# Optimization experiments

Measured on AMD Instinct MI355X. Metric: run time of the kernel, lower is better.

## Reference

```python
import jax, jax.numpy as jnp
import numpy as np


def setup_inputs() -> dict:
    key = jax.random.key(0)
    k1, k2 = jax.random.split(key)
    B, Q, T, D = 128, 512, 512, 256
    inputs = jax.random.normal(k1, (B, T, D), dtype=jnp.float32)
    query = jax.random.normal(k2, (B, Q, D), dtype=jnp.float32)
    return {"inputs": inputs, "query": query}


def reference(inputs, query):
    # inputs: [B, T, D] (keys == values), query: [B, Q, D]
    D = inputs.shape[2]
    scale = 1.0 / jnp.sqrt(jnp.asarray(D, dtype=inputs.dtype))
    # scores: [B, Q, T]
    scores = jnp.einsum("bqd,btd->bqt", query, inputs) * scale
    weights = jax.nn.softmax(scores, axis=2)
    # attended: [B, Q, D]
    attended = jnp.einsum("bqt,btd->bqd", weights, inputs)
    # pool over query dim -> [B, D]
    return jnp.sum(attended, axis=1)
```

## Files before the change

### kernel.cpp

```cpp
#include <hip/hip_runtime.h>
#include <hip/hip_bf16.h>


typedef __bf16 bf16x8 __attribute__((ext_vector_type(8)));
typedef float  f32x4  __attribute__((ext_vector_type(4)));

#define B_    128
#define Tn    512
#define Dn    256
#define SCALE 0.0625f

__device__ __forceinline__ int lidx(int row, int ch) {
  return row * 256 + (((ch ^ (row & 31)) & 31) << 3);
}

__device__ __forceinline__ void stage_load(const float* __restrict__ src,
                                           int tid, float4* pre) {
#pragma unroll
  for (int i = 0; i < 8; ++i) {
    int u = i * 256 + tid;
    int row = u >> 5, ch = u & 31;
    const float4* p = (const float4*)(src + row * 256 + ch * 8);
    pre[2 * i]     = p[0];
    pre[2 * i + 1] = p[1];
  }
}

__device__ __forceinline__ void stage_store(__bf16* dst, int tid,
                                            const float4* pre) {
#pragma unroll
  for (int i = 0; i < 8; ++i) {
    int u = i * 256 + tid;
    int row = u >> 5, ch = u & 31;
    float4 v0 = pre[2 * i], v1 = pre[2 * i + 1];
    bf16x8 w;
    w[0] = (__bf16)v0.x; w[1] = (__bf16)v0.y;
    w[2] = (__bf16)v0.z; w[3] = (__bf16)v0.w;
    w[4] = (__bf16)v1.x; w[5] = (__bf16)v1.y;
    w[6] = (__bf16)v1.z; w[7] = (__bf16)v1.w;
    *(bf16x8*)(dst + lidx(row, ch)) = w;
  }
}

__global__ void __launch_bounds__(256, 2) attn_qk_colsum(
    const float* __restrict__ inputs, const float* __restrict__ query,
    float* __restrict__ c_ws) {
  __shared__ __bf16 smem[2 * 64 * 256];
  __bf16* buf0 = smem;
  __bf16* buf1 = smem + 64 * 256;

  const int tid  = threadIdx.x;
  const int bidx = blockIdx.x;
  const int b  = bidx & 127;
  const int qt = bidx >> 7;

  const float* qsrc = query  + ((size_t)b * 512 + (size_t)qt * 64) * Dn;
  const float* ksrc = inputs + (size_t)b * Tn * Dn;

  const int wave = tid >> 6, lane = tid & 63;
  const int quad = lane >> 4, l15 = lane & 15;
  const int qh = wave & 1;
  const int th = wave >> 1;

  {
    float4 pre[16];
    stage_load(qsrc, tid, pre);
    stage_store(buf0, tid, pre);
  }
  __syncthreads();

  bf16x8 afrag[2][8];
#pragma unroll
  for (int m = 0; m < 2; ++m)
#pragma unroll
    for (int dc = 0; dc < 8; ++dc)
      afrag[m][dc] =
          *(const bf16x8*)(buf0 + lidx(qh * 32 + m * 16 + l15, dc * 4 + quad));

  {
    float4 pre[16];
    stage_load(ksrc, tid, pre);
    stage_store(buf1, tid, pre);
  }
  __syncthreads();

  f32x4 acc[8][2][2];
  f32x4 zero = {0.f, 0.f, 0.f, 0.f};
#pragma unroll
  for (int tt = 0; tt < 8; ++tt)
#pragma unroll
    for (int ct = 0; ct < 2; ++ct) {
      acc[tt][ct][0] = zero;
      acc[tt][ct][1] = zero;
    }

#pragma unroll
  for (int tt = 0; tt < 8; ++tt) {
    __bf16* cur = (tt & 1) ? buf0 : buf1;
    __bf16* nxt = (tt & 1) ? buf1 : buf0;
    float4 pre[16];
    if (tt < 7) stage_load(ksrc + (size_t)(tt + 1) * 64 * Dn, tid, pre);
#pragma unroll
    for (int dc = 0; dc < 8; ++dc) {
#pragma unroll
      for (int ct = 0; ct < 2; ++ct) {
        bf16x8 bb =
            *(const bf16x8*)(cur + lidx(th * 32 + ct * 16 + l15, dc * 4 + quad));
        acc[tt][ct][0] = __builtin_amdgcn_mfma_f32_16x16x32_bf16(
            afrag[0][dc], bb, acc[tt][ct][0], 0, 0, 0);
        acc[tt][ct][1] = __builtin_amdgcn_mfma_f32_16x16x32_bf16(
            afrag[1][dc], bb, acc[tt][ct][1], 0, 0, 0);
      }
    }
    if (tt < 7) stage_store(nxt, tid, pre);
    __syncthreads();
  }

#pragma unroll
  for (int tt = 0; tt < 8; ++tt)
#pragma unroll
    for (int ct = 0; ct < 2; ++ct)
#pragma unroll
      for (int m = 0; m < 2; ++m)
#pragma unroll
        for (int r = 0; r < 4; ++r)
          acc[tt][ct][m][r] = __expf(acc[tt][ct][m][r] * SCALE);

  float rs[2][4];
#pragma unroll
  for (int m = 0; m < 2; ++m)
#pragma unroll
    for (int r = 0; r < 4; ++r) rs[m][r] = 0.f;
#pragma unroll
  for (int tt = 0; tt < 8; ++tt)
#pragma unroll
    for (int ct = 0; ct < 2; ++ct)
#pragma unroll
      for (int m = 0; m < 2; ++m)
#pragma unroll
        for (int r = 0; r < 4; ++r) rs[m][r] += acc[tt][ct][m][r];
#pragma unroll
  for (int off = 1; off <= 8; off <<= 1)
#pragma unroll
    for (int m = 0; m < 2; ++m)
#pragma unroll
      for (int r = 0; r < 4; ++r) rs[m][r] += __shfl_xor(rs[m][r], off);

  float* lhalf = (float*)smem;
  if (l15 == 0) {
#pragma unroll
    for (int m = 0; m < 2; ++m)
#pragma unroll
      for (int r = 0; r < 4; ++r)
        lhalf[(qh * 2 + th) * 32 + m * 16 + quad * 4 + r] = rs[m][r];
  }
  __syncthreads();

  float linv[2][4];
#pragma unroll
  for (int m = 0; m < 2; ++m)
#pragma unroll
    for (int r = 0; r < 4; ++r) {
      int row = m * 16 + quad * 4 + r;
      linv[m][r] =
          1.f / (lhalf[(qh * 2 + 0) * 32 + row] + lhalf[(qh * 2 + 1) * 32 + row]);
    }

  float* cwave = (float*)smem + 128;
#pragma unroll
  for (int tt = 0; tt < 8; ++tt)
#pragma unroll
    for (int ct = 0; ct < 2; ++ct) {
      float v = 0.f;
#pragma unroll
      for (int m = 0; m < 2; ++m)
#pragma unroll
        for (int r = 0; r < 4; ++r) v += acc[tt][ct][m][r] * linv[m][r];
      v += __shfl_xor(v, 16);
      v += __shfl_xor(v, 32);
      if (quad == 0)
        cwave[qh * 512 + tt * 64 + th * 32 + ct * 16 + l15] = v;
    }
  __syncthreads();

  float* cout = c_ws + ((size_t)qt * B_ + b) * Tn;
#pragma unroll
  for (int t = tid; t < 512; t += 256) cout[t] = cwave[t] + cwave[512 + t];
}

__global__ void __launch_bounds__(256) attn_av(
    const float* __restrict__ inputs, const float* __restrict__ c_ws,
    float* __restrict__ out) {
  __shared__ float ctot[128];
  __shared__ float psum[3][256];
  const int bid = blockIdx.x, tid = threadIdx.x;
  const int b = bid & 127, tq = bid >> 7;

  if (tid < 128) {
    float s = 0.f;
#pragma unroll
    for (int q = 0; q < 8; ++q)
      s += c_ws[(size_t)(q * B_ + b) * Tn + tq * 128 + tid];
    ctot[tid] = s;
  }
  __syncthreads();

  const int d4 = tid & 63;
  const int ts = tid >> 6;
  const float4* vb =
      (const float4*)(inputs + ((size_t)b * Tn + tq * 128 + ts * 32) * Dn) + d4;
  float4 o = {0.f, 0.f, 0.f, 0.f};
#pragma unroll
  for (int j = 0; j < 32; ++j) {
    float c = ctot[ts * 32 + j];
    float4 v = vb[(size_t)j * 64];
    o.x += c * v.x; o.y += c * v.y; o.z += c * v.z; o.w += c * v.w;
  }
  if (ts) *(float4*)&psum[ts - 1][d4 * 4] = o;
  __syncthreads();
  if (!ts) {
    float4 p0 = *(float4*)&psum[0][d4 * 4];
    float4 p1 = *(float4*)&psum[1][d4 * 4];
    float4 p2 = *(float4*)&psum[2][d4 * 4];
    o.x += p0.x + p1.x + p2.x;
    o.y += p0.y + p1.y + p2.y;
    o.z += p0.z + p1.z + p2.z;
    o.w += p0.w + p1.w + p2.w;
    float* op = out + b * 256 + d4 * 4;
    atomicAdd(op + 0, o.x);
    atomicAdd(op + 1, o.y);
    atomicAdd(op + 2, o.z);
    atomicAdd(op + 3, o.w);
  }
}

extern "C" void kernel_launch(void* const* d_in, const int* in_sizes, int n_in,
                              void* d_out, int out_size, void* d_ws, size_t ws_size,
                              hipStream_t stream) {
  const float* inputs = (const float*)d_in[0];
  const float* query  = (const float*)d_in[1];
  float* out  = (float*)d_out;
  float* c_ws = (float*)d_ws;

  hipMemsetAsync(out, 0, (size_t)B_ * Dn * sizeof(float), stream);
  attn_qk_colsum<<<dim3(1024), dim3(256), 0, stream>>>(inputs, query, c_ws);
  attn_av<<<dim3(512), dim3(256), 0, stream>>>(inputs, c_ws, out);
}
```

Baseline: 183.0 us.

## Use 128-query tiles with 512-thread blocks and atomically accumulate column sums

The QK kernel now processes 128 queries per block with 8 waves sharing each staged K tile. This halves the number of blocks that re-read and convert the K matrix. The per-query-tile column sums are accumulated into a single workspace with atomics, so the AV kernel reads one vector instead of summing eight partials. The AV kernel is split into more, smaller blocks. The changes add an extra memset, atomics on the column-sum buffer, and a larger shared memory footprint that may reduce occupancy.

```diff
diff --git a/kernel.cpp b/kernel.cpp
--- a/kernel.cpp
+++ b/kernel.cpp
@@ -14,11 +14,11 @@
   return row * 256 + (((ch ^ (row & 31)) & 31) << 3);
 }
 
-__device__ __forceinline__ void stage_load(const float* __restrict__ src,
-                                           int tid, float4* pre) {
-#pragma unroll
-  for (int i = 0; i < 8; ++i) {
-    int u = i * 256 + tid;
+__device__ __forceinline__ void kload(const float* __restrict__ src, int tid,
+                                      float4* pre) {
+#pragma unroll
+  for (int i = 0; i < 4; ++i) {
+    int u = i * 512 + tid;
     int row = u >> 5, ch = u & 31;
     const float4* p = (const float4*)(src + row * 256 + ch * 8);
     pre[2 * i]     = p[0];
@@ -26,11 +26,11 @@
   }
 }
 
-__device__ __forceinline__ void stage_store(__bf16* dst, int tid,
-                                            const float4* pre) {
-#pragma unroll
-  for (int i = 0; i < 8; ++i) {
-    int u = i * 256 + tid;
+__device__ __forceinline__ void kstore(__bf16* dst, int tid,
+                                       const float4* pre) {
+#pragma unroll
+  for (int i = 0; i < 4; ++i) {
+    int u = i * 512 + tid;
     int row = u >> 5, ch = u & 31;
     float4 v0 = pre[2 * i], v1 = pre[2 * i + 1];
     bf16x8 w;
@@ -42,31 +42,41 @@
   }
 }
 
-__global__ void __launch_bounds__(256, 2) attn_qk_colsum(
+__global__ void __launch_bounds__(512, 2) attn_qk(
     const float* __restrict__ inputs, const float* __restrict__ query,
-    float* __restrict__ c_ws) {
-  __shared__ __bf16 smem[2 * 64 * 256];
-  __bf16* buf0 = smem;
-  __bf16* buf1 = smem + 64 * 256;
+    float* __restrict__ c_tot) {
+  __shared__ __bf16 Qs[128 * 256];
+  __shared__ __bf16 Ks[2][64 * 256];
 
   const int tid  = threadIdx.x;
   const int bidx = blockIdx.x;
   const int b  = bidx & 127;
   const int qt = bidx >> 7;
 
-  const float* qsrc = query  + ((size_t)b * 512 + (size_t)qt * 64) * Dn;
+  const float* qsrc = query  + ((size_t)b * 512 + (size_t)qt * 128) * Dn;
   const float* ksrc = inputs + (size_t)b * Tn * Dn;
 
   const int wave = tid >> 6, lane = tid & 63;
   const int quad = lane >> 4, l15 = lane & 15;
-  const int qh = wave & 1;
-  const int th = wave >> 1;
-
-  {
-    float4 pre[16];
-    stage_load(qsrc, tid, pre);
-    stage_store(buf0, tid, pre);
-  }
+  const int qg = wave >> 1;
+  const int th = wave & 1;
+
+#pragma unroll
+  for (int i = 0; i < 8; ++i) {
+    int u = i * 512 + tid;
+    int row = u >> 5, ch = u & 31;
+    const float4* p = (const float4*)(qsrc + row * 256 + ch * 8);
+    float4 v0 = p[0], v1 = p[1];
+    bf16x8 w;
+    w[0] = (__bf16)v0.x; w[1] = (__bf16)v0.y;
+    w[2] = (__bf16)v0.z; w[3] = (__bf16)v0.w;
+    w[4] = (__bf16)v1.x; w[5] = (__bf16)v1.y;
+    w[6] = (__bf16)v1.z; w[7] = (__bf16)v1.w;
+    *(bf16x8*)(Qs + lidx(row, ch)) = w;
+  }
+
+  float4 pre[8];
+  kload(ksrc, tid, pre);
   __syncthreads();
 
   bf16x8 afrag[2][8];
@@ -75,13 +85,9 @@
 #pragma unroll
     for (int dc = 0; dc < 8; ++dc)
       afrag[m][dc] =
-          *(const bf16x8*)(buf0 + lidx(qh * 32 + m * 16 + l15, dc * 4 + quad));
-
-  {
-    float4 pre[16];
-    stage_load(ksrc, tid, pre);
-    stage_store(buf1, tid, pre);
-  }
+          *(const bf16x8*)(Qs + lidx(qg * 32 + m * 16 + l15, dc * 4 + quad));
+
+  kstore(Ks[0], tid, pre);
   __syncthreads();
 
   f32x4 acc[8][2][2];
@@ -96,10 +102,8 @@
 
 #pragma unroll
   for (int tt = 0; tt < 8; ++tt) {
-    __bf16* cur = (tt & 1) ? buf0 : buf1;
-    __bf16* nxt = (tt & 1) ? buf1 : buf0;
-    float4 pre[16];
-    if (tt < 7) stage_load(ksrc + (size_t)(tt + 1) * 64 * Dn, tid, pre);
+    if (tt < 7) kload(ksrc + (size_t)(tt + 1) * 64 * Dn, tid, pre);
+    const __bf16* cur = Ks[tt & 1];
 #pragma unroll
     for (int dc = 0; dc < 8; ++dc) {
 #pragma unroll
@@ -112,10 +116,18 @@
             afrag[1][dc], bb, acc[tt][ct][1], 0, 0, 0);
       }
     }
-    if (tt < 7) stage_store(nxt, tid, pre);
+    if (tt < 7) kstore((__bf16*)Ks[(tt + 1) & 1], tid, pre);
     __syncthreads();
   }
 
+  float* lred  = (float*)Ks[0];
+  float* cpart = (float*)Ks[0] + 256;
+
+  float rs[2][4];
+#pragma unroll
+  for (int m = 0; m < 2; ++m)
+#pragma unroll
+    for (int r = 0; r < 4; ++r) rs[m][r] = 0.f;
 #pragma unroll
   for (int tt = 0; tt < 8; ++tt)
 #pragma unroll
@@ -123,22 +135,11 @@
 #pragma unroll
       for (int m = 0; m < 2; ++m)
 #pragma unroll
-        for (int r = 0; r < 4; ++r)
-          acc[tt][ct][m][r] = __expf(acc[tt][ct][m][r] * SCALE);
-
-  float rs[2][4];
-#pragma unroll
-  for (int m = 0; m < 2; ++m)
-#pragma unroll
-    for (int r = 0; r < 4; ++r) rs[m][r] = 0.f;
-#pragma unroll
-  for (int tt = 0; tt < 8; ++tt)
-#pragma unroll
-    for (int ct = 0; ct < 2; ++ct)
-#pragma unroll
-      for (int m = 0; m < 2; ++m)
-#pragma unroll
-        for (int r = 0; r < 4; ++r) rs[m][r] += acc[tt][ct][m][r];
+        for (int r = 0; r < 4; ++r) {
+          float p = __expf(acc[tt][ct][m][r] * SCALE);
+          acc[tt][ct][m][r] = p;
+          rs[m][r] += p;
+        }
 #pragma unroll
   for (int off = 1; off <= 8; off <<= 1)
 #pragma unroll
@@ -146,13 +147,12 @@
 #pragma unroll
       for (int r = 0; r < 4; ++r) rs[m][r] += __shfl_xor(rs[m][r], off);
 
-  float* lhalf = (float*)smem;
   if (l15 == 0) {
 #pragma unroll
     for (int m = 0; m < 2; ++m)
 #pragma unroll
       for (int r = 0; r < 4; ++r)
-        lhalf[(qh * 2 + th) * 32 + m * 16 + quad * 4 + r] = rs[m][r];
+        lred[(qg * 2 + th) * 32 + m * 16 + quad * 4 + r] = rs[m][r];
   }
   __syncthreads();
 
@@ -163,10 +163,9 @@
     for (int r = 0; r < 4; ++r) {
       int row = m * 16 + quad * 4 + r;
       linv[m][r] =
-          1.f / (lhalf[(qh * 2 + 0) * 32 + row] + lhalf[(qh * 2 + 1) * 32 + row]);
-    }
-
-  float* cwave = (float*)smem + 128;
+          1.f / (lred[(qg * 2 + 0) * 32 + row] + lred[(qg * 2 + 1) * 32 + row]);
+    }
+
 #pragma unroll
   for (int tt = 0; tt < 8; ++tt)
 #pragma unroll
@@ -179,58 +178,49 @@
       v += __shfl_xor(v, 16);
       v += __shfl_xor(v, 32);
       if (quad == 0)
-        cwave[qh * 512 + tt * 64 + th * 32 + ct * 16 + l15] = v;
-    }
-  __syncthreads();
-
-  float* cout = c_ws + ((size_t)qt * B_ + b) * Tn;
-#pragma unroll
-  for (int t = tid; t < 512; t += 256) cout[t] = cwave[t] + cwave[512 + t];
+        cpart[qg * 512 + tt * 64 + th * 32 + ct * 16 + l15] = v;
+    }
+  __syncthreads();
+
+  float c = cpart[tid] + cpart[512 + tid] + cpart[1024 + tid] + cpart[1536 + tid];
+  atomicAdd(c_tot + (size_t)b * Tn + tid, c);
 }
 
 __global__ void __launch_bounds__(256) attn_av(
-    const float* __restrict__ inputs, const float* __restrict__ c_ws,
+    const float* __restrict__ inputs, const float* __restrict__ c_tot,
     float* __restrict__ out) {
-  __shared__ float ctot[128];
+  __shared__ float cs[64];
   __shared__ float psum[3][256];
   const int bid = blockIdx.x, tid = threadIdx.x;
-  const int b = bid & 127, tq = bid >> 7;
-
-  if (tid < 128) {
-    float s = 0.f;
-#pragma unroll
-    for (int q = 0; q < 8; ++q)
-      s += c_ws[(size_t)(q * B_ + b) * Tn + tq * 128 + tid];
-    ctot[tid] = s;
-  }
-  __syncthreads();
-
-  const int d4 = tid & 63;
-  const int ts = tid >> 6;
+  const int b = bid & 127, sl = bid >> 7;
+
+  if (tid < 64) cs[tid] = c_tot[(size_t)b * Tn + sl * 64 + tid];
+  __syncthreads();
+
+  const int w = tid >> 6, d4 = tid & 63;
   const float4* vb =
-      (const float4*)(inputs + ((size_t)b * Tn + tq * 128 + ts * 32) * Dn) + d4;
-  float4 o = {0.f, 0.f, 0.f, 0.f};
-#pragma unroll
-  for (int j = 0; j < 32; ++j) {
-    float c = ctot[ts * 32 + j];
+      (const float4*)(inputs + ((size_t)b * Tn + sl * 64 + w * 16) * Dn) + d4;
+  float ox = 0.f, oy = 0.f, oz = 0.f, ow = 0.f;
+#pragma unroll
+  for (int j = 0; j < 16; ++j) {
+    float c = cs[w * 16 + j];
     float4 v = vb[(size_t)j * 64];
-    o.x += c * v.x; o.y += c * v.y; o.z += c * v.z; o.w += c * v.w;
-  }
-  if (ts) *(float4*)&psum[ts - 1][d4 * 4] = o;
-  __syncthreads();
-  if (!ts) {
+    ox += c * v.x; oy += c * v.y; oz += c * v.z; ow += c * v.w;
+  }
+  if (w) {
+    float4 t = {ox, oy, oz, ow};
+    *(float4*)&psum[w - 1][d4 * 4] = t;
+  }
+  __syncthreads();
+  if (!w) {
     float4 p0 = *(float4*)&psum[0][d4 * 4];
     float4 p1 = *(float4*)&psum[1][d4 * 4];
     float4 p2 = *(float4*)&psum[2][d4 * 4];
-    o.x += p0.x + p1.x + p2.x;
-    o.y += p0.y + p1.y + p2.y;
-    o.z += p0.z + p1.z + p2.z;
-    o.w += p0.w + p1.w + p2.w;
     float* op = out + b * 256 + d4 * 4;
-    atomicAdd(op + 0, o.x);
-    atomicAdd(op + 1, o.y);
-    atomicAdd(op + 2, o.z);
-    atomicAdd(op + 3, o.w);
+    atomicAdd(op + 0, ox + p0.x + p1.x + p2.x);
+    atomicAdd(op + 1, oy + p0.y + p1.y + p2.y);
+    atomicAdd(op + 2, oz + p0.z + p1.z + p2.z);
+    atomicAdd(op + 3, ow + p0.w + p1.w + p2.w);
   }
 }
 
@@ -239,10 +229,11 @@
                               hipStream_t stream) {
   const float* inputs = (const float*)d_in[0];
   const float* query  = (const float*)d_in[1];
-  float* out  = (float*)d_out;
-  float* c_ws = (float*)d_ws;
+  float* out   = (float*)d_out;
+  float* c_tot = (float*)d_ws;
 
   hipMemsetAsync(out, 0, (size_t)B_ * Dn * sizeof(float), stream);
-  attn_qk_colsum<<<dim3(1024), dim3(256), 0, stream>>>(inputs, query, c_ws);
-  attn_av<<<dim3(512), dim3(256), 0, stream>>>(inputs, c_ws, out);
-}
+  hipMemsetAsync(c_tot, 0, (size_t)B_ * Tn * sizeof(float), stream);
+  attn_qk<<<dim3(512), dim3(512), 0, stream>>>(inputs, query, c_tot);
+  attn_av<<<dim3(1024), dim3(256), 0, stream>>>(inputs, c_tot, out);
+}
```

New measurement: 183.9 us. No clear change (+0.5%).
